# Optimization experiments

Measured on AMD Instinct MI355X. Metric: run time of the kernel, lower is better.

The kernel has to match this reference:

```python
import jax, jax.numpy as jnp
import numpy as np

N = 40000      # total nodes in the batched graph
E = 640000     # total edges (avg degree 16)
F_IN = 1280    # num_features (ESM embedding dim)
H = 128        # hidden_dim
G = 64         # number of graphs in the batch
OUT = 273      # output_dim (GO terms)
NEG_SLOPE = 0.2
BN_EPS = 1e-5


def setup_inputs() -> dict:
    key = jax.random.key(0)
    ks = jax.random.split(key, 16)
    def nrm(k, shape, s=0.05):
        return jax.random.normal(k, shape, dtype=jnp.float32) * s
    inp = {}
    inp["x"] = jax.random.normal(ks[0], (N, F_IN), dtype=jnp.float32)
    inp["edge_index"] = jax.random.randint(ks[1], (2, E), 0, N, dtype=jnp.int32)
    inp["batch"] = jnp.sort(jax.random.randint(ks[2], (N,), 0, G, dtype=jnp.int32))
    inp["W1"] = nrm(ks[3], (F_IN, H)); inp["b1"] = jnp.zeros((H,), jnp.float32)
    inp["a_src1"] = nrm(ks[4], (H,)); inp["a_dst1"] = nrm(ks[5], (H,))
    inp["W2"] = nrm(ks[6], (H, H)); inp["b2"] = jnp.zeros((H,), jnp.float32)
    inp["a_src2"] = nrm(ks[7], (H,)); inp["a_dst2"] = nrm(ks[8], (H,))
    inp["W3"] = nrm(ks[9], (H, H)); inp["b3"] = jnp.zeros((H,), jnp.float32)
    inp["a_src3"] = nrm(ks[10], (H,)); inp["a_dst3"] = nrm(ks[11], (H,))
    inp["fc1_W"] = nrm(ks[12], (H, 1024)); inp["fc1_b"] = jnp.zeros((1024,), jnp.float32)
    inp["bn_g"] = jnp.ones((1024,), jnp.float32); inp["bn_b"] = jnp.zeros((1024,), jnp.float32)
    inp["bn_rm"] = jnp.zeros((1024,), jnp.float32); inp["bn_rv"] = jnp.ones((1024,), jnp.float32)
    inp["fc2_W"] = nrm(ks[13], (1024, OUT)); inp["fc2_b"] = jnp.zeros((OUT,), jnp.float32)
    return inp


def gat_layer(x, W, b, a_src, a_dst, src, dst, n_nodes):
    # single-head GAT ('gat_originated'): h = xW, e_ij = lrelu(a_src.h_j + a_dst.h_i)
    h = x @ W                                            # [N, H]
    e = jax.nn.leaky_relu((h @ a_src)[src] + (h @ a_dst)[dst], NEG_SLOPE)  # [E]
    # numerically-stable segment softmax over incoming edges of each target node
    m = jax.ops.segment_max(e, dst, num_segments=n_nodes)
    p = jnp.exp(e - m[dst])
    denom = jax.ops.segment_sum(p, dst, num_segments=n_nodes)
    alpha = p / (denom[dst] + 1e-16)                     # [E]
    out = jax.ops.segment_sum(alpha[:, None] * h[src], dst, num_segments=n_nodes)
    return out + b


def reference(x, edge_index, batch, W1, b1, a_src1, a_dst1, W2, b2, a_src2, a_dst2,
              W3, b3, a_src3, a_dst3, fc1_W, fc1_b, bn_g, bn_b, bn_rm, bn_rv, fc2_W, fc2_b):
    n = x.shape[0]
    src, dst = edge_index[0], edge_index[1]
    h = jax.nn.relu(gat_layer(x, W1, b1, a_src1, a_dst1, src, dst, n))
    h = jax.nn.relu(gat_layer(h, W2, b2, a_src2, a_dst2, src, dst, n))
    h = gat_layer(h, W3, b3, a_src3, a_dst3, src, dst, n)
    # gap: global mean pool per graph
    cnt = jax.ops.segment_sum(jnp.ones((n,), h.dtype), batch, num_segments=G)
    pooled = jax.ops.segment_sum(h, batch, num_segments=G) / jnp.maximum(cnt, 1.0)[:, None]
    z = pooled @ fc1_W + fc1_b                            # [G, 1024]
    z = (z - bn_rm) * jax.lax.rsqrt(bn_rv + BN_EPS) * bn_g + bn_b  # BN eval mode
    z = jax.nn.relu(z)                                    # dropout is identity in eval
    return jax.nn.sigmoid(z @ fc2_W + fc2_b)              # [G, 273]
```

## Files before the change

kernel.cpp:

```cpp
#include <hip/hip_runtime.h>
#include <math.h>

#define N_NODES 40000
#define N_EDGES 640000
#define F_IN    1280
#define H       128
#define NG      64
#define OUTD    273
#define FC1D    1024
#define NEG_SLOPE 0.2f
#define BN_EPS  1e-5f

typedef __attribute__((ext_vector_type(8))) short short8;
typedef __attribute__((ext_vector_type(4))) float f32x4;

__device__ __forceinline__ unsigned short f2bf(float f) {
    unsigned u = __float_as_uint(f);
    u += 0x7FFF + ((u >> 16) & 1);
    return (unsigned short)(u >> 16);
}
__device__ __forceinline__ float bf2f(unsigned short s) {
    return __uint_as_float((unsigned)s << 16);
}

__global__ void edge_hist(const int* __restrict__ dst, int* __restrict__ cnt, int e) {
    int i = blockIdx.x * blockDim.x + threadIdx.x;
    if (i < e) atomicAdd(&cnt[dst[i]], 1);
}

__global__ void scan_excl(const int* __restrict__ cnt, int* __restrict__ row_ptr, int n) {
    const int CH = 40;
    __shared__ int sm[1024];
    int tid = threadIdx.x;
    int start = tid * CH;
    int local[CH];
    int s = 0;
    #pragma unroll
    for (int k = 0; k < CH; ++k) {
        int i = start + k;
        int v = (i < n) ? cnt[i] : 0;
        local[k] = s;
        s += v;
    }
    sm[tid] = s;
    __syncthreads();
    for (int off = 1; off < 1024; off <<= 1) {
        int t = (tid >= off) ? sm[tid - off] : 0;
        __syncthreads();
        sm[tid] += t;
        __syncthreads();
    }
    int base = sm[tid] - s;
    #pragma unroll
    for (int k = 0; k < CH; ++k) {
        int i = start + k;
        if (i < n) row_ptr[i] = base + local[k];
    }
    if (tid == 1023) row_ptr[n] = sm[1023];
}

__global__ void edge_fill(const int* __restrict__ src, const int* __restrict__ dst,
                          const int* __restrict__ row_ptr, int* __restrict__ fill,
                          int* __restrict__ csr_src, int e) {
    int i = blockIdx.x * blockDim.x + threadIdx.x;
    if (i < e) {
        int d = dst[i];
        int pos = row_ptr[d] + atomicAdd(&fill[d], 1);
        csr_src[pos] = src[i];
    }
}

__global__ void wprep(const float* __restrict__ W, unsigned short* __restrict__ Bp, int K) {
    int i = blockIdx.x * blockDim.x + threadIdx.x;
    if (i >= K * H) return;
    int k = i >> 7, col = i & 127;
    float v = W[i];
    unsigned short hh = f2bf(v);
    unsigned short ll = f2bf(v - bf2f(hh));
    int t = k >> 6, rr = k & 63;
    int s = rr >> 5, r5 = rr & 31;
    int laneHi = r5 >> 3, j = r5 & 7;
    int lane = laneHi * 16 + (col & 15);
    int n = col >> 4;
    int U = (n * 2 + s) * 64 + lane;
    size_t idx = (size_t)t * 16384 + (size_t)U * 8 + j;
    Bp[idx] = hh;
    Bp[idx + 8192] = ll;
}

__device__ __forceinline__ void cvt8(float4 x, float4 y, short8& hi, short8& lo) {
    float f[8] = {x.x, x.y, x.z, x.w, y.x, y.y, y.z, y.w};
    #pragma unroll
    for (int j = 0; j < 8; ++j) {
        unsigned u = __float_as_uint(f[j]);
        unsigned short hh = (unsigned short)((u + 0x7FFF + ((u >> 16) & 1)) >> 16);
        hi[j] = (short)hh;
        float r = f[j] - __uint_as_float((unsigned)hh << 16);
        unsigned ur = __float_as_uint(r);
        lo[j] = (short)((ur + 0x7FFF + ((ur >> 16) & 1)) >> 16);
    }
}

__global__ __launch_bounds__(256) void gemm_mfma(
    const float* __restrict__ A, const unsigned short* __restrict__ Bp,
    float* __restrict__ C, int K)
{
    __shared__ __align__(16) unsigned short lds[16384];
    const int tid  = threadIdx.x;
    const int lane = tid & 63, wv = tid >> 6;
    const int fr = lane & 15, q = lane >> 4;
    const int m0 = blockIdx.x * 64;
    const int row = m0 + wv * 16 + fr;
    const int nt = K >> 6;

    const uint4* gb = (const uint4*)Bp + tid;
    uint4* lp = (uint4*)lds + tid;

    uint4 f0 = gb[0],    f1 = gb[256],  f2 = gb[512],  f3 = gb[768],
          f4 = gb[1024], f5 = gb[1280], f6 = gb[1536], f7 = gb[1792];

    f32x4 acc0 = {}, acc1 = {}, acc2 = {}, acc3 = {},
          acc4 = {}, acc5 = {}, acc6 = {}, acc7 = {};

    for (int t = 0; t < nt; ++t) {
        lp[0] = f0;    lp[256] = f1;  lp[512] = f2;  lp[768] = f3;
        lp[1024] = f4; lp[1280] = f5; lp[1536] = f6; lp[1792] = f7;
        if (t + 1 < nt) {
            const uint4* g = gb + (size_t)(t + 1) * 2048;
            f0 = g[0];    f1 = g[256];  f2 = g[512];  f3 = g[768];
            f4 = g[1024]; f5 = g[1280]; f6 = g[1536]; f7 = g[1792];
        }
        __syncthreads();

        const float* ap = A + (size_t)row * K + t * 64 + q * 8;
        float4 a0 = *(const float4*)(ap);
        float4 a1 = *(const float4*)(ap + 4);
        float4 a2 = *(const float4*)(ap + 32);
        float4 a3 = *(const float4*)(ap + 36);

        short8 ah, al;
#define MSTEP(nn, accv, ss)                                                     \
        {                                                                       \
            const short8 bh = *(const short8*)&lds[(size_t)(((nn)*2+(ss))*64 + lane)*8];          \
            const short8 bl = *(const short8*)&lds[(size_t)(((nn)*2+(ss))*64 + lane)*8 + 8192];   \
            accv = __builtin_amdgcn_mfma_f32_16x16x32_bf16(ah, bh, accv, 0, 0, 0);                \
            accv = __builtin_amdgcn_mfma_f32_16x16x32_bf16(ah, bl, accv, 0, 0, 0);                \
            accv = __builtin_amdgcn_mfma_f32_16x16x32_bf16(al, bh, accv, 0, 0, 0);                \
        }
        cvt8(a0, a1, ah, al);
        MSTEP(0, acc0, 0) MSTEP(1, acc1, 0) MSTEP(2, acc2, 0) MSTEP(3, acc3, 0)
        MSTEP(4, acc4, 0) MSTEP(5, acc5, 0) MSTEP(6, acc6, 0) MSTEP(7, acc7, 0)
        cvt8(a2, a3, ah, al);
        MSTEP(0, acc0, 1) MSTEP(1, acc1, 1) MSTEP(2, acc2, 1) MSTEP(3, acc3, 1)
        MSTEP(4, acc4, 1) MSTEP(5, acc5, 1) MSTEP(6, acc6, 1) MSTEP(7, acc7, 1)
#undef MSTEP
        __syncthreads();
    }

    const int rb = m0 + wv * 16 + q * 4;
#define EPI(nn, accv)                                                           \
    {                                                                           \
        _Pragma("unroll")                                                       \
        for (int i = 0; i < 4; ++i)                                             \
            C[(size_t)(rb + i) * H + (nn)*16 + fr] = accv[i];                   \
    }
    EPI(0, acc0) EPI(1, acc1) EPI(2, acc2) EPI(3, acc3)
    EPI(4, acc4) EPI(5, acc5) EPI(6, acc6) EPI(7, acc7)
#undef EPI
}

__global__ void scores_k(const float* __restrict__ h, const float* __restrict__ a_s,
                         const float* __restrict__ a_d, float* __restrict__ hs,
                         float* __restrict__ hd, int n) {
    int wv = (blockIdx.x * blockDim.x + threadIdx.x) >> 6;
    int lane = threadIdx.x & 63;
    if (wv >= n) return;
    float v0 = h[(size_t)wv * H + lane];
    float v1 = h[(size_t)wv * H + 64 + lane];
    float s = v0 * a_s[lane] + v1 * a_s[64 + lane];
    float d = v0 * a_d[lane] + v1 * a_d[64 + lane];
    #pragma unroll
    for (int off = 32; off; off >>= 1) {
        s += __shfl_xor(s, off);
        d += __shfl_xor(d, off);
    }
    if (lane == 0) { hs[wv] = s; hd[wv] = d; }
}

__global__ void attn_agg(const float* __restrict__ h, const float* __restrict__ hs,
                         const float* __restrict__ hd, const int* __restrict__ row_ptr,
                         const int* __restrict__ csr_src, const float* __restrict__ bias,
                         float* __restrict__ out, int n, int relu_flag) {
    int wv = (blockIdx.x * blockDim.x + threadIdx.x) >> 6;
    int lane = threadIdx.x & 63;
    if (wv >= n) return;
    int p0 = row_ptr[wv], p1 = row_ptr[wv + 1];
    int deg = p1 - p0;
    float hdi = hd[wv];
    float ax = 0.f, ay = 0.f;

    if (deg <= 64) {
        int valid = (lane < deg);
        int sidx = valid ? csr_src[p0 + lane] : 0;
        float e = hs[sidx] + hdi;
        e = (e >= 0.f) ? e : NEG_SLOPE * e;
        float ev = valid ? e : -3.4e38f;
        float m = ev;
        #pragma unroll
        for (int off = 32; off; off >>= 1) m = fmaxf(m, __shfl_xor(m, off));
        float pe = valid ? __expf(e - m) : 0.f;
        float dsum = pe;
        #pragma unroll
        for (int off = 32; off; off >>= 1) dsum += __shfl_xor(dsum, off);
        pe *= 1.f / (dsum + 1e-16f);
        for (int j = 0; j < deg; ++j) {
            float alpha = __shfl(pe, j);
            int s = __shfl(sidx, j);
            float2 hv = *(const float2*)&h[(size_t)s * H + 2 * lane];
            ax += alpha * hv.x;
            ay += alpha * hv.y;
        }
    } else {
        float m = -3.4e38f;
        for (int p = p0 + lane; p < p1; p += 64) {
            float e = hs[csr_src[p]] + hdi;
            e = (e >= 0.f) ? e : NEG_SLOPE * e;
            m = fmaxf(m, e);
        }
        #pragma unroll
        for (int off = 32; off; off >>= 1) m = fmaxf(m, __shfl_xor(m, off));
        float dsum = 0.f;
        for (int p = p0 + lane; p < p1; p += 64) {
            float e = hs[csr_src[p]] + hdi;
            e = (e >= 0.f) ? e : NEG_SLOPE * e;
            dsum += __expf(e - m);
        }
        #pragma unroll
        for (int off = 32; off; off >>= 1) dsum += __shfl_xor(dsum, off);
        float inv = 1.f / (dsum + 1e-16f);
        for (int p = p0; p < p1; ++p) {
            int s = csr_src[p];
            float e = hs[s] + hdi;
            e = (e >= 0.f) ? e : NEG_SLOPE * e;
            float alpha = __expf(e - m) * inv;
            float2 hv = *(const float2*)&h[(size_t)s * H + 2 * lane];
            ax += alpha * hv.x;
            ay += alpha * hv.y;
        }
    }
    float2 bv = *(const float2*)&bias[2 * lane];
    float o0 = ax + bv.x;
    float o1 = ay + bv.y;
    if (relu_flag) { o0 = fmaxf(o0, 0.f); o1 = fmaxf(o1, 0.f); }
    float2 ov; ov.x = o0; ov.y = o1;
    *(float2*)&out[(size_t)wv * H + 2 * lane] = ov;
}

__device__ __forceinline__ void graph_range(const int* __restrict__ batch, int n,
                                            int g, int& start, int& end) {
    int lo = 0, hi = n;
    while (lo < hi) { int mid = (lo + hi) >> 1; if (batch[mid] < g) lo = mid + 1; else hi = mid; }
    start = lo;
    lo = start; hi = n;
    while (lo < hi) { int mid = (lo + hi) >> 1; if (batch[mid] < g + 1) lo = mid + 1; else hi = mid; }
    end = lo;
}

__global__ void pool_part(const float* __restrict__ h, const int* __restrict__ batch,
                          float* __restrict__ part, int n) {
    int g = blockIdx.x >> 3, c = blockIdx.x & 7;
    int f = threadIdx.x;
    int start, end;
    graph_range(batch, n, g, start, end);
    int len = end - start;
    int cs = start + (len * c) / 8, ce = start + (len * (c + 1)) / 8;
    float acc = 0.f;
    for (int i = cs; i < ce; ++i) acc += h[(size_t)i * H + f];
    part[((size_t)g * 8 + c) * H + f] = acc;
}

__global__ void pool_final(const float* __restrict__ part, const int* __restrict__ batch,
                           float* __restrict__ pooled, int n) {
    int g = blockIdx.x;
    int f = threadIdx.x;
    int start, end;
    graph_range(batch, n, g, start, end);
    float s = 0.f;
    #pragma unroll
    for (int c = 0; c < 8; ++c) s += part[((size_t)g * 8 + c) * H + f];
    float cnt = (float)(end - start);
    pooled[g * H + f] = s / fmaxf(cnt, 1.f);
}

__global__ void fc1_bn_relu(const float* __restrict__ pooled, const float* __restrict__ W,
                            const float* __restrict__ b, const float* __restrict__ bng,
                            const float* __restrict__ bnb, const float* __restrict__ bnrm,
                            const float* __restrict__ bnrv, float* __restrict__ z) {
    int g = blockIdx.x >> 2;
    int j = ((blockIdx.x & 3) << 8) + threadIdx.x;
    const float* pr = pooled + g * H;
    float acc = b[j];
    #pragma unroll 8
    for (int k = 0; k < H; ++k) acc += pr[k] * W[k * FC1D + j];
    float v = (acc - bnrm[j]) * rsqrtf(bnrv[j] + BN_EPS) * bng[j] + bnb[j];
    z[g * FC1D + j] = fmaxf(v, 0.f);
}

__global__ void fc2_sig(const float* __restrict__ z, const float* __restrict__ W,
                        const float* __restrict__ b, float* __restrict__ out) {
    int g = blockIdx.x;
    int j = threadIdx.x;
    if (j >= OUTD) return;
    const float* zr = z + g * FC1D;
    float acc = b[j];
    #pragma unroll 4
    for (int k = 0; k < FC1D; ++k) acc += zr[k] * W[k * OUTD + j];
    out[g * OUTD + j] = 1.f / (1.f + __expf(-acc));
}

extern "C" void kernel_launch(void* const* d_in, const int* in_sizes, int n_in,
                              void* d_out, int out_size, void* d_ws, size_t ws_size,
                              hipStream_t stream) {
    const float* x     = (const float*)d_in[0];
    const int*   eidx  = (const int*)d_in[1];
    const int*   batch = (const int*)d_in[2];
    const float* W1 = (const float*)d_in[3];  const float* b1 = (const float*)d_in[4];
    const float* as1 = (const float*)d_in[5]; const float* ad1 = (const float*)d_in[6];
    const float* W2 = (const float*)d_in[7];  const float* b2 = (const float*)d_in[8];
    const float* as2 = (const float*)d_in[9]; const float* ad2 = (const float*)d_in[10];
    const float* W3 = (const float*)d_in[11]; const float* b3 = (const float*)d_in[12];
    const float* as3 = (const float*)d_in[13]; const float* ad3 = (const float*)d_in[14];
    const float* fc1W = (const float*)d_in[15]; const float* fc1b = (const float*)d_in[16];
    const float* bng = (const float*)d_in[17];  const float* bnb = (const float*)d_in[18];
    const float* bnrm = (const float*)d_in[19]; const float* bnrv = (const float*)d_in[20];
    const float* fc2W = (const float*)d_in[21]; const float* fc2b = (const float*)d_in[22];
    const int* src = eidx;
    const int* dst = eidx + N_EDGES;

    float* hW      = (float*)d_ws;
    float* hA      = hW + (size_t)N_NODES * H;
    float* hs      = hA + (size_t)N_NODES * H;
    float* hd      = hs + N_NODES;
    int*   row_ptr = (int*)(hd + N_NODES);
    int*   row_cnt = row_ptr + (N_NODES + 1);
    int*   csr_src = row_cnt + N_NODES;
    float* pooled  = (float*)(csr_src + N_EDGES);
    float* part    = pooled + NG * H;
    float* z       = part + NG * 8 * H;
    unsigned short* Bp1 = (unsigned short*)(z + NG * FC1D);
    unsigned short* Bp2 = Bp1 + (size_t)(F_IN / 64) * 16384;
    unsigned short* Bp3 = Bp2 + (size_t)(H / 64) * 16384;

    const int EB = (N_EDGES + 255) / 256;
    const int NW = (N_NODES * 64 + 255) / 256;
    const int GB = N_NODES / 64;

    wprep<<<(F_IN * H + 255) / 256, 256, 0, stream>>>(W1, Bp1, F_IN);
    wprep<<<(H * H + 255) / 256, 256, 0, stream>>>(W2, Bp2, H);
    wprep<<<(H * H + 255) / 256, 256, 0, stream>>>(W3, Bp3, H);

    hipMemsetAsync(row_cnt, 0, N_NODES * sizeof(int), stream);
    edge_hist<<<EB, 256, 0, stream>>>(dst, row_cnt, N_EDGES);
    scan_excl<<<1, 1024, 0, stream>>>(row_cnt, row_ptr, N_NODES);
    hipMemsetAsync(row_cnt, 0, N_NODES * sizeof(int), stream);
    edge_fill<<<EB, 256, 0, stream>>>(src, dst, row_ptr, row_cnt, csr_src, N_EDGES);

    gemm_mfma<<<GB, 256, 0, stream>>>(x, Bp1, hW, F_IN);
    scores_k<<<NW, 256, 0, stream>>>(hW, as1, ad1, hs, hd, N_NODES);
    attn_agg<<<NW, 256, 0, stream>>>(hW, hs, hd, row_ptr, csr_src, b1, hA, N_NODES, 1);
    gemm_mfma<<<GB, 256, 0, stream>>>(hA, Bp2, hW, H);
    scores_k<<<NW, 256, 0, stream>>>(hW, as2, ad2, hs, hd, N_NODES);
    attn_agg<<<NW, 256, 0, stream>>>(hW, hs, hd, row_ptr, csr_src, b2, hA, N_NODES, 1);
    gemm_mfma<<<GB, 256, 0, stream>>>(hA, Bp3, hW, H);
    scores_k<<<NW, 256, 0, stream>>>(hW, as3, ad3, hs, hd, N_NODES);
    attn_agg<<<NW, 256, 0, stream>>>(hW, hs, hd, row_ptr, csr_src, b3, hA, N_NODES, 0);

    pool_part<<<NG * 8, H, 0, stream>>>(hA, batch, part, N_NODES);
    pool_final<<<NG, H, 0, stream>>>(part, batch, pooled, N_NODES);
    fc1_bn_relu<<<NG * 4, 256, 0, stream>>>(pooled, fc1W, fc1b, bng, bnb, bnrm, bnrv, z);
    fc2_sig<<<NG, 320, 0, stream>>>(z, fc2W, fc2b, (float*)d_out);
}
```

Measured before the change: 834.0 us.

## Fuse attention scores into GEMM epilogue and store projected features as bf16

Computes the per-node source and destination attention scores inside the MFMA GEMM epilogue from the accumulators, which removes the separate scores kernel and its re-read of the projected features. The projected features are now written as bf16, halving the bytes fetched in the gather-heavy aggregation. The aggregation loop is also unrolled by four so several row gathers are in flight at once. The cost is reduced precision in the aggregated features.

```diff
diff --git a/kernel.cpp b/kernel.cpp
--- a/kernel.cpp
+++ b/kernel.cpp
@@ -101,9 +101,11 @@
     }
 }
 
-__global__ __launch_bounds__(256) void gemm_mfma(
+__global__ __launch_bounds__(256) void gemm_fused(
     const float* __restrict__ A, const unsigned short* __restrict__ Bp,
-    float* __restrict__ C, int K)
+    const float* __restrict__ a_src, const float* __restrict__ a_dst,
+    unsigned short* __restrict__ hWb, float* __restrict__ hs,
+    float* __restrict__ hd, int K)
 {
     __shared__ __align__(16) unsigned short lds[16384];
     const int tid  = threadIdx.x;
@@ -162,35 +164,41 @@
     {                                                                           \
         _Pragma("unroll")                                                       \
         for (int i = 0; i < 4; ++i)                                             \
-            C[(size_t)(rb + i) * H + (nn)*16 + fr] = accv[i];                   \
+            hWb[(size_t)(rb + i) * H + (nn)*16 + fr] = f2bf(accv[i]);           \
     }
     EPI(0, acc0) EPI(1, acc1) EPI(2, acc2) EPI(3, acc3)
     EPI(4, acc4) EPI(5, acc5) EPI(6, acc6) EPI(7, acc7)
 #undef EPI
-}
-
-__global__ void scores_k(const float* __restrict__ h, const float* __restrict__ a_s,
-                         const float* __restrict__ a_d, float* __restrict__ hs,
-                         float* __restrict__ hd, int n) {
-    int wv = (blockIdx.x * blockDim.x + threadIdx.x) >> 6;
-    int lane = threadIdx.x & 63;
-    if (wv >= n) return;
-    float v0 = h[(size_t)wv * H + lane];
-    float v1 = h[(size_t)wv * H + 64 + lane];
-    float s = v0 * a_s[lane] + v1 * a_s[64 + lane];
-    float d = v0 * a_d[lane] + v1 * a_d[64 + lane];
-    #pragma unroll
-    for (int off = 32; off; off >>= 1) {
-        s += __shfl_xor(s, off);
-        d += __shfl_xor(d, off);
-    }
-    if (lane == 0) { hs[wv] = s; hd[wv] = d; }
-}
-
-__global__ void attn_agg(const float* __restrict__ h, const float* __restrict__ hs,
-                         const float* __restrict__ hd, const int* __restrict__ row_ptr,
-                         const int* __restrict__ csr_src, const float* __restrict__ bias,
-                         float* __restrict__ out, int n, int relu_flag) {
+
+    float asv[8], adv[8];
+    #pragma unroll
+    for (int n = 0; n < 8; ++n) {
+        asv[n] = a_src[n * 16 + fr];
+        adv[n] = a_dst[n * 16 + fr];
+    }
+    #pragma unroll
+    for (int i = 0; i < 4; ++i) {
+        float ss = acc0[i]*asv[0] + acc1[i]*asv[1] + acc2[i]*asv[2] + acc3[i]*asv[3]
+                 + acc4[i]*asv[4] + acc5[i]*asv[5] + acc6[i]*asv[6] + acc7[i]*asv[7];
+        float dd = acc0[i]*adv[0] + acc1[i]*adv[1] + acc2[i]*adv[2] + acc3[i]*adv[3]
+                 + acc4[i]*adv[4] + acc5[i]*adv[5] + acc6[i]*adv[6] + acc7[i]*adv[7];
+        #pragma unroll
+        for (int off = 8; off; off >>= 1) {
+            ss += __shfl_xor(ss, off);
+            dd += __shfl_xor(dd, off);
+        }
+        if (fr == 0) { hs[rb + i] = ss; hd[rb + i] = dd; }
+    }
+}
+
+__device__ __forceinline__ float bfhi(unsigned u) { return __uint_as_float(u << 16); }
+__device__ __forceinline__ float bflo(unsigned u) { return __uint_as_float(u & 0xffff0000u); }
+
+__global__ void attn_agg(const unsigned short* __restrict__ hWb,
+                         const float* __restrict__ hs, const float* __restrict__ hd,
+                         const int* __restrict__ row_ptr, const int* __restrict__ csr_src,
+                         const float* __restrict__ bias, float* __restrict__ out,
+                         int n, int relu_flag) {
     int wv = (blockIdx.x * blockDim.x + threadIdx.x) >> 6;
     int lane = threadIdx.x & 63;
     if (wv >= n) return;
@@ -198,6 +206,7 @@
     int deg = p1 - p0;
     float hdi = hd[wv];
     float ax = 0.f, ay = 0.f;
+    const unsigned* hb = (const unsigned*)hWb;
 
     if (deg <= 64) {
         int valid = (lane < deg);
@@ -213,12 +222,28 @@
         #pragma unroll
         for (int off = 32; off; off >>= 1) dsum += __shfl_xor(dsum, off);
         pe *= 1.f / (dsum + 1e-16f);
-        for (int j = 0; j < deg; ++j) {
+
+        int j = 0;
+        int dq = deg & ~3;
+        for (; j < dq; j += 4) {
+            float al0 = __shfl(pe, j),     al1 = __shfl(pe, j + 1);
+            float al2 = __shfl(pe, j + 2), al3 = __shfl(pe, j + 3);
+            int s0 = __shfl(sidx, j),     s1 = __shfl(sidx, j + 1);
+            int s2 = __shfl(sidx, j + 2), s3 = __shfl(sidx, j + 3);
+            unsigned u0 = hb[(size_t)s0 * 64 + lane];
+            unsigned u1 = hb[(size_t)s1 * 64 + lane];
+            unsigned u2 = hb[(size_t)s2 * 64 + lane];
+            unsigned u3 = hb[(size_t)s3 * 64 + lane];
+            ax += al0 * bfhi(u0); ay += al0 * bflo(u0);
+            ax += al1 * bfhi(u1); ay += al1 * bflo(u1);
+            ax += al2 * bfhi(u2); ay += al2 * bflo(u2);
+            ax += al3 * bfhi(u3); ay += al3 * bflo(u3);
+        }
+        for (; j < deg; ++j) {
             float alpha = __shfl(pe, j);
             int s = __shfl(sidx, j);
-            float2 hv = *(const float2*)&h[(size_t)s * H + 2 * lane];
-            ax += alpha * hv.x;
-            ay += alpha * hv.y;
+            unsigned u = hb[(size_t)s * 64 + lane];
+            ax += alpha * bfhi(u); ay += alpha * bflo(u);
         }
     } else {
         float m = -3.4e38f;
@@ -243,9 +268,8 @@
             float e = hs[s] + hdi;
             e = (e >= 0.f) ? e : NEG_SLOPE * e;
             float alpha = __expf(e - m) * inv;
-            float2 hv = *(const float2*)&h[(size_t)s * H + 2 * lane];
-            ax += alpha * hv.x;
-            ay += alpha * hv.y;
+            unsigned u = hb[(size_t)s * 64 + lane];
+            ax += alpha * bfhi(u); ay += alpha * bflo(u);
         }
     }
     float2 bv = *(const float2*)&bias[2 * lane];
@@ -337,19 +361,19 @@
     const int* src = eidx;
     const int* dst = eidx + N_EDGES;
 
-    float* hW      = (float*)d_ws;
-    float* hA      = hW + (size_t)N_NODES * H;
+    float* hA      = (float*)d_ws;
     float* hs      = hA + (size_t)N_NODES * H;
     float* hd      = hs + N_NODES;
-    int*   row_ptr = (int*)(hd + N_NODES);
+    float* pooled  = hd + N_NODES;
+    float* part    = pooled + NG * H;
+    float* z       = part + NG * 8 * H;
+    unsigned short* hWb = (unsigned short*)(z + NG * FC1D);
+    unsigned short* Bp1 = hWb + (size_t)N_NODES * H;
+    unsigned short* Bp2 = Bp1 + (size_t)(F_IN / 64) * 16384;
+    unsigned short* Bp3 = Bp2 + (size_t)(H / 64) * 16384;
+    int*   row_ptr = (int*)(Bp3 + (size_t)(H / 64) * 16384);
     int*   row_cnt = row_ptr + (N_NODES + 1);
     int*   csr_src = row_cnt + N_NODES;
-    float* pooled  = (float*)(csr_src + N_EDGES);
-    float* part    = pooled + NG * H;
-    float* z       = part + NG * 8 * H;
-    unsigned short* Bp1 = (unsigned short*)(z + NG * FC1D);
-    unsigned short* Bp2 = Bp1 + (size_t)(F_IN / 64) * 16384;
-    unsigned short* Bp3 = Bp2 + (size_t)(H / 64) * 16384;
 
     const int EB = (N_EDGES + 255) / 256;
     const int NW = (N_NODES * 64 + 255) / 256;
@@ -365,15 +389,12 @@
     hipMemsetAsync(row_cnt, 0, N_NODES * sizeof(int), stream);
     edge_fill<<<EB, 256, 0, stream>>>(src, dst, row_ptr, row_cnt, csr_src, N_EDGES);
 
-    gemm_mfma<<<GB, 256, 0, stream>>>(x, Bp1, hW, F_IN);
-    scores_k<<<NW, 256, 0, stream>>>(hW, as1, ad1, hs, hd, N_NODES);
-    attn_agg<<<NW, 256, 0, stream>>>(hW, hs, hd, row_ptr, csr_src, b1, hA, N_NODES, 1);
-    gemm_mfma<<<GB, 256, 0, stream>>>(hA, Bp2, hW, H);
-    scores_k<<<NW, 256, 0, stream>>>(hW, as2, ad2, hs, hd, N_NODES);
-    attn_agg<<<NW, 256, 0, stream>>>(hW, hs, hd, row_ptr, csr_src, b2, hA, N_NODES, 1);
-    gemm_mfma<<<GB, 256, 0, stream>>>(hA, Bp3, hW, H);
-    scores_k<<<NW, 256, 0, stream>>>(hW, as3, ad3, hs, hd, N_NODES);
-    attn_agg<<<NW, 256, 0, stream>>>(hW, hs, hd, row_ptr, csr_src, b3, hA, N_NODES, 0);
+    gemm_fused<<<GB, 256, 0, stream>>>(x, Bp1, as1, ad1, hWb, hs, hd, F_IN);
+    attn_agg<<<NW, 256, 0, stream>>>(hWb, hs, hd, row_ptr, csr_src, b1, hA, N_NODES, 1);
+    gemm_fused<<<GB, 256, 0, stream>>>(hA, Bp2, as2, ad2, hWb, hs, hd, H);
+    attn_agg<<<NW, 256, 0, stream>>>(hWb, hs, hd, row_ptr, csr_src, b2, hA, N_NODES, 1);
+    gemm_fused<<<GB, 256, 0, stream>>>(hA, Bp3, as3, ad3, hWb, hs, hd, H);
+    attn_agg<<<NW, 256, 0, stream>>>(hWb, hs, hd, row_ptr, csr_src, b3, hA, N_NODES, 0);
 
     pool_part<<<NG * 8, H, 0, stream>>>(hA, batch, part, N_NODES);
     pool_final<<<NG, H, 0, stream>>>(part, batch, pooled, N_NODES);
```

After: 744.9 us. 1.12x faster.
